# Optimization experiments

Measured on AMD Instinct MI355X. Metric: run time of the kernel, lower is better.

## Reference

```python
import jax, jax.numpy as jnp
import numpy as np
from math import factorial

N_NODES = 10000
N_EDGES = 320000
FEAT = 32
NBASIS = 8
RMAX = 6.0
ZMAX = 119


def _cg(j1, m1, j2, m2, j3, m3):
    if m1 + m2 != m3 or j3 < abs(j1 - j2) or j3 > j1 + j2:
        return 0.0
    f = lambda n: float(factorial(n))
    pre = ((2 * j3 + 1) * f(j1 + j2 - j3) * f(j1 - j2 + j3) * f(-j1 + j2 + j3) / f(j1 + j2 + j3 + 1)) ** 0.5
    pre *= (f(j3 + m3) * f(j3 - m3) * f(j1 - m1) * f(j1 + m1) * f(j2 - m2) * f(j2 + m2)) ** 0.5
    s = 0.0
    for k in range(j1 + j2 + j3 + 1):
        d = [k, j1 + j2 - j3 - k, j1 - m1 - k, j2 + m2 - k, j3 - j2 + m1 + k, j3 - j1 - m2 + k]
        if min(d) < 0:
            continue
        s += (-1) ** k / (f(d[0]) * f(d[1]) * f(d[2]) * f(d[3]) * f(d[4]) * f(d[5]))
    return pre * s


def _u_real(l):
    # complex->real spherical harmonics unitary transform
    U = np.zeros((2 * l + 1, 2 * l + 1), dtype=complex)
    s2 = 1.0 / np.sqrt(2.0)
    for m in range(-l, l + 1):
        i = m + l
        if m == 0:
            U[i, l] = 1.0
        elif m > 0:
            U[i, l + m] = ((-1) ** m) * s2
            U[i, l - m] = s2
        else:
            U[i, l + m] = 1j * s2
            U[i, l - m] = -1j * ((-1) ** m) * s2
    return U


def _real_cg():
    # real Clebsch-Gordan coupling coefficients for l<=2, shape (9,9,9), sparse
    off = [0, 1, 4]
    C = np.zeros((9, 9, 9))
    Us = [_u_real(l) for l in range(3)]
    for l1 in range(3):
        for l2 in range(3):
            for l3 in range(3):
                if l3 < abs(l1 - l2) or l3 > l1 + l2:
                    continue
                cg = np.zeros((2 * l1 + 1, 2 * l2 + 1, 2 * l3 + 1))
                for m1 in range(-l1, l1 + 1):
                    for m2 in range(-l2, l2 + 1):
                        m3 = m1 + m2
                        if abs(m3) <= l3:
                            cg[m1 + l1, m2 + l2, m3 + l3] = _cg(l1, m1, l2, m2, l3, m3)
                blk = np.einsum('ia,jb,kc,abc->ijk', Us[l1], Us[l2], np.conj(Us[l3]), cg.astype(complex))
                C[off[l1]:off[l1] + 2 * l1 + 1, off[l2]:off[l2] + 2 * l2 + 1, off[l3]:off[l3] + 2 * l3 + 1] = blk.real + blk.imag
    return C

CGC = jnp.asarray(_real_cg(), dtype=jnp.float32)
SL = [slice(0, 1), slice(1, 4), slice(4, 9)]
PATHS0 = [(0, 0, 0), (0, 1, 1), (0, 2, 2)]
PATHS1 = [(l1, l2, l3) for l1 in range(3) for l2 in range(3) for l3 in range(3) if abs(l1 - l2) <= l3 <= l1 + l2]
PATHS2 = [(0, 0, 0), (1, 1, 0), (2, 2, 0)]


def _real_sph(u):
    x, y, z = u[:, 0], u[:, 1], u[:, 2]
    c0 = 0.28209479177387814
    c1 = 0.4886025119029199
    c2a = 1.0925484305920792
    c2b = 0.31539156525252005
    c2c = 0.5462742152960396
    return jnp.stack([c0 * jnp.ones_like(x), c1 * y, c1 * z, c1 * x,
                      c2a * x * y, c2a * y * z, c2b * (3.0 * z * z - 1.0), c2a * x * z,
                      c2c * (x * x - y * y)], axis=-1)


def _message_pass(x, rad, Y, src, dst, W, paths, out_dim, n_nodes):
    # gather src node features -> per-edge CG tensor product with (radial x Ylm) basis -> scatter-add to dst
    xs = x[src, 0]  # (E, Dx, F)
    msg = jnp.zeros((rad.shape[0], out_dim, x.shape[-1]), x.dtype)
    for p, (l1, l2, l3) in enumerate(paths):
        w = rad @ W[p]  # (E, F) learned radial path weights
        contrib = jnp.einsum('abc,eaf,eb,ef->ecf', CGC[SL[l1], SL[l2], SL[l3]], xs[:, SL[l1], :], Y[:, SL[l2]], w)
        msg = msg.at[:, SL[l3], :].add(contrib)
    y = jax.ops.segment_sum(msg, dst, num_segments=n_nodes)
    return y[:, None]  # (N, 1, out_dim, F)


def _eadd(a, b):
    if a.shape[2] == b.shape[2]:
        return a + b
    if a.shape[2] < b.shape[2]:
        a, b = b, a
    return a.at[:, :, :b.shape[2], :].add(b)


def _edense(x, K, b):
    # equivariant Dense: shared kernel across degrees, bias only on scalar (l=0) channel
    y = jnp.einsum('npdf,fg->npdg', x, K)
    return y.at[:, :, 0, :].add(b)


def _esilu(x):
    # silu on scalars, sigmoid(scalar)-gated scaling on l>0 components (equivariant)
    if x.shape[2] == 1:
        return jax.nn.silu(x)
    s = x[:, :, 0:1, :]
    return jnp.concatenate([jax.nn.silu(s), x[:, :, 1:, :] * jax.nn.sigmoid(s)], axis=2)


def _forward(dr_vec, Z, neighbor_idxs, embed, wmp0, wmp1, wmp2, dk1, db1, dk2, db2):
    idx_i, idx_j = neighbor_idxs[0], neighbor_idxs[1]
    nN = Z.shape[0]
    r = jnp.sqrt(jnp.sum(dr_vec * dr_vec, axis=-1) + 1e-12)  # (E,)
    u = dr_vec / r[:, None]
    n = jnp.arange(1, NBASIS + 1, dtype=dr_vec.dtype)
    rad = jnp.sqrt(2.0 / RMAX) * jnp.sin(n * jnp.pi * r[:, None] / RMAX) / r[:, None]  # Bessel radial basis
    t = jnp.clip(r / RMAX, 0.0, 1.0 - 1e-6)
    cut = jnp.where(r < RMAX, jnp.exp(1.0 - 1.0 / (1.0 - t * t)), 0.0)  # smooth cutoff
    mask = (idx_i != idx_j).astype(dr_vec.dtype)  # mask padding/self edges
    rad = rad * (cut * mask)[:, None]
    Y = _real_sph(u)  # (E, 9)
    x = embed[Z][:, None, None, :]  # (N, 1, 1, F)
    for it, (paths, W) in enumerate([(PATHS0, wmp0), (PATHS1, wmp1), (PATHS2, wmp2)]):
        last = it == 2
        y = _message_pass(x, rad, Y, idx_j, idx_i, W, paths, 1 if last else 9, nN)
        if last:
            x = x[:, :, 0:1, :]  # change_max_degree_or_type -> scalars only
        y = _eadd(x, y)
        y = _edense(y, dk1[it], db1[it])
        y = _esilu(y)
        y = _edense(y, dk2[it], db2[it])
        x = _eadd(x, y)
    return x[:, 0, 0, :]


def setup_inputs():
    key = jax.random.key(0)
    ks = jax.random.split(key, 10)
    dr_vec = 2.0 * jax.random.normal(ks[0], (N_EDGES, 3), jnp.float32)
    Z = jax.random.randint(ks[1], (N_NODES,), 0, ZMAX)
    neighbor_idxs = jax.random.randint(ks[2], (2, N_EDGES), 0, N_NODES)
    embed = jax.random.normal(ks[3], (ZMAX, FEAT), jnp.float32)
    sB = 1.0 / np.sqrt(NBASIS)
    wmp0 = sB * jax.random.normal(ks[4], (len(PATHS0), NBASIS, FEAT), jnp.float32)
    wmp1 = sB * jax.random.normal(ks[5], (len(PATHS1), NBASIS, FEAT), jnp.float32)
    wmp2 = sB * jax.random.normal(ks[6], (len(PATHS2), NBASIS, FEAT), jnp.float32)
    sF = 1.0 / np.sqrt(FEAT)
    dense_k1 = sF * jax.random.normal(ks[7], (3, FEAT, FEAT), jnp.float32)
    dense_b1 = jnp.zeros((3, FEAT), jnp.float32)
    dense_k2 = 0.1 * sF * jax.random.normal(ks[8], (3, FEAT, FEAT), jnp.float32)
    dense_b2 = jnp.zeros((3, FEAT), jnp.float32)
    return {"dr_vec": dr_vec, "Z": Z, "neighbor_idxs": neighbor_idxs, "embed": embed,
            "wmp0": wmp0, "wmp1": wmp1, "wmp2": wmp2,
            "dense_k1": dense_k1, "dense_b1": dense_b1, "dense_k2": dense_k2, "dense_b2": dense_b2}


def reference(dr_vec, Z, neighbor_idxs, embed, wmp0, wmp1, wmp2, dense_k1, dense_b1, dense_k2, dense_b2):
    return _forward(dr_vec, Z, neighbor_idxs, embed, wmp0, wmp1, wmp2, dense_k1, dense_b1, dense_k2, dense_b2)
```

## Files before the change

kernel.cpp:

```cpp
#include <hip/hip_runtime.h>
#include <type_traits>
#include <cstdint>
#include <cstddef>

#define N_FEAT 32
#define NBASIS 8
#define SPAN   16
#define BSLOTS 8
#define BEDGES (SPAN*BSLOTS)

namespace cgc {

constexpr double dfact(int n){ double r=1.0; for(int i=2;i<=n;++i) r*=(double)i; return r; }

constexpr double dsqrt(double x){
  if(x<=0.0) return 0.0;
  double g = x>1.0 ? x : 1.0;
  for(int i=0;i<200;++i){ double ng = 0.5*(g + x/g); if(ng==g) break; g=ng; }
  return g;
}

constexpr double cg1(int j1,int m1,int j2,int m2,int j3,int m3){
  int adiff = j1-j2; if(adiff<0) adiff=-adiff;
  if(m1+m2!=m3 || j3<adiff || j3>j1+j2) return 0.0;
  double pre = dsqrt((double)(2*j3+1)*dfact(j1+j2-j3)*dfact(j1-j2+j3)*dfact(-j1+j2+j3)/dfact(j1+j2+j3+1));
  pre = pre*dsqrt(dfact(j3+m3)*dfact(j3-m3)*dfact(j1-m1)*dfact(j1+m1)*dfact(j2-m2)*dfact(j2+m2));
  double s=0.0;
  for(int k=0;k<=j1+j2+j3;++k){
    int d1=j1+j2-j3-k, d2=j1-m1-k, d3=j2+m2-k, d4=j3-j2+m1+k, d5=j3-j1-m2+k;
    if(d1<0||d2<0||d3<0||d4<0||d5<0) continue;
    double term = 1.0/(dfact(k)*dfact(d1)*dfact(d2)*dfact(d3)*dfact(d4)*dfact(d5));
    s += (k&1)? -term : term;
  }
  return pre*s;
}

struct Tab { float v[9][9][9]; };

constexpr Tab make(){
  Tab T{};
  int off[3]={0,1,4};
  double Ure[3][5][5]={}, Uim[3][5][5]={};
  const double s2 = dsqrt(0.5);
  for(int l=0;l<3;++l){
    for(int m=-l;m<=l;++m){
      int i=m+l;
      if(m==0){ Ure[l][i][l]=1.0; }
      else if(m>0){
        Ure[l][i][l+m] = ((m&1)? -1.0:1.0)*s2;
        Ure[l][i][l-m] = s2;
      } else {
        int am=-m;
        Uim[l][i][l+m] = s2;
        Uim[l][i][l-m] = -(((am&1)?-1.0:1.0))*s2;
      }
    }
  }
  for(int l1=0;l1<3;++l1) for(int l2=0;l2<3;++l2) for(int l3=0;l3<3;++l3){
    int lo = l1-l2; if(lo<0) lo=-lo;
    if(l3<lo || l3>l1+l2) continue;
    int d1=2*l1+1, d2=2*l2+1, d3=2*l3+1;
    double cg[5][5][5]={};
    for(int m1=-l1;m1<=l1;++m1) for(int m2=-l2;m2<=l2;++m2){
      int m3=m1+m2;
      if(m3>=-l3 && m3<=l3) cg[m1+l1][m2+l2][m3+l3] = cg1(l1,m1,l2,m2,l3,m3);
    }
    double t1re[5][5][5]={}, t1im[5][5][5]={};
    for(int a=0;a<d1;++a) for(int b=0;b<d2;++b) for(int k=0;k<d3;++k){
      double sre=0, sim=0;
      for(int c=0;c<d3;++c){
        double g=cg[a][b][c]; if(g==0.0) continue;
        sre += g*Ure[l3][k][c];
        sim -= g*Uim[l3][k][c];
      }
      t1re[a][b][k]=sre; t1im[a][b][k]=sim;
    }
    double t2re[5][5][5]={}, t2im[5][5][5]={};
    for(int a=0;a<d1;++a) for(int j=0;j<d2;++j) for(int k=0;k<d3;++k){
      double sre=0,sim=0;
      for(int b=0;b<d2;++b){
        double ur=Ure[l2][j][b], ui=Uim[l2][j][b];
        if(ur==0.0&&ui==0.0) continue;
        sre += ur*t1re[a][b][k]-ui*t1im[a][b][k];
        sim += ur*t1im[a][b][k]+ui*t1re[a][b][k];
      }
      t2re[a][j][k]=sre; t2im[a][j][k]=sim;
    }
    for(int i=0;i<d1;++i) for(int j=0;j<d2;++j) for(int k=0;k<d3;++k){
      double sre=0,sim=0;
      for(int a=0;a<d1;++a){
        double ur=Ure[l1][i][a], ui=Uim[l1][i][a];
        if(ur==0.0&&ui==0.0) continue;
        sre += ur*t2re[a][j][k]-ui*t2im[a][j][k];
        sim += ur*t2im[a][j][k]+ui*t2re[a][j][k];
      }
      T.v[off[l1]+i][off[l2]+j][off[l3]+k] = (float)(sre+sim);
    }
  }
  return T;
}

constexpr Tab T = make();

}

template<int I, int N, typename F>
__device__ __forceinline__ void sfor(F&& f){
  if constexpr (I < N){
    f(std::integral_constant<int,I>{});
    sfor<I+1,N>(static_cast<F&&>(f));
  }
}

constexpr int LOFF[3] = {0,1,4};

struct PS0 {
  static constexpr int NP=3;
  static constexpr int L[3][3]={{0,0,0},{0,1,1},{0,2,2}};
  static constexpr int ALO=0, AHI=1, OD=9, WOFF=0;
  static constexpr int MINW=4, DEPTH=8;
};
struct PS1a {
  static constexpr int NP=9;
  static constexpr int L[9][3]={{0,0,0},{0,1,1},{0,2,2},
                                {1,0,1},{1,1,0},{1,1,1},{1,1,2},{1,2,1},{1,2,2}};
  static constexpr int ALO=0, AHI=4, OD=9, WOFF=0;
  static constexpr int MINW=3, DEPTH=3;
};
struct PS1b {
  static constexpr int NP=6;
  static constexpr int L[6][3]={{2,0,2},{2,1,1},{2,1,2},{2,2,0},{2,2,1},{2,2,2}};
  static constexpr int ALO=4, AHI=9, OD=9, WOFF=9*NBASIS*N_FEAT;
  static constexpr int MINW=3, DEPTH=3;
};
struct PS2 {
  static constexpr int NP=3;
  static constexpr int L[3][3]={{0,0,0},{1,1,0},{2,2,0}};
  static constexpr int ALO=0, AHI=9, OD=1, WOFF=0;
  static constexpr int MINW=3, DEPTH=3;
};

__global__ void init_kernel(const float* __restrict__ embed, const int* __restrict__ Z,
                            float* __restrict__ xA, int* __restrict__ cnt, int nN){
  int i = blockIdx.x*256 + threadIdx.x;
  if(i >= nN*N_FEAT) return;
  int n = i>>5, f = i&31;
  if(f==0) cnt[n]=0;
  xA[(size_t)n*288 + f] = embed[Z[n]*N_FEAT + f];
}

__global__ void count_kernel(const int* __restrict__ dst, int* __restrict__ cnt, int E){
  int e = blockIdx.x*256 + threadIdx.x;
  if(e<E) atomicAdd(&cnt[dst[e]], 1);
}

__global__ void __launch_bounds__(1024) scan_kernel(const int* __restrict__ cnt,
                                                    int* __restrict__ cursor, int n){
  __shared__ int part[1024];
  const int tid = threadIdx.x;
  const int chunk = (n + 1023) >> 10;
  const int s0 = tid*chunk;
  const int s1 = (s0+chunk < n) ? s0+chunk : n;
  int s=0;
  for(int i=s0;i<s1;++i) s += cnt[i];
  part[tid]=s; __syncthreads();
  for(int off=1; off<1024; off<<=1){
    int v = 0;
    if(tid>=off) v = part[tid-off];
    __syncthreads();
    part[tid] += v;
    __syncthreads();
  }
  int run = part[tid] - s;
  for(int i=s0;i<s1;++i){
    int cv = cnt[i];
    cursor[i]=run;
    run += cv;
  }
}

__global__ void fillgeom_kernel(const int* __restrict__ dst, const int* __restrict__ src,
                                const float* __restrict__ dr, int* __restrict__ cursor,
                                int* __restrict__ srcsP, float* __restrict__ radY, int E){
  int e = blockIdx.x*256 + threadIdx.x;
  if(e>=E) return;
  const int d = dst[e], s = src[e];
  const int pos = atomicAdd(&cursor[d], 1);
  srcsP[pos] = s | (d<<16);

  float dx=dr[3*e], dy=dr[3*e+1], dz=dr[3*e+2];
  float r2 = fmaf(dx,dx,fmaf(dy,dy,fmaf(dz,dz,1e-12f)));
  float r = sqrtf(r2);
  float inv = 1.f/r;
  float ux=dx*inv, uy=dy*inv, uz=dz*inv;
  float t = r*(1.f/6.f);
  t = fminf(fmaxf(t,0.f), 1.f-1e-6f);
  float cut = 0.f;
  if (r < 6.f) cut = __expf(1.f - 1.f/(1.f - t*t));
  if (d==s) cut = 0.f;
  float base = 0.57735026918962576f * inv * cut;
  float* o = radY + (size_t)pos*20;
  const float pir = 0.52359877559829887f * r;
  float sT, cT;
  __sincosf(pir, &sT, &cT);
  const float twoc = 2.f*cT;
  float sp = 0.f, sc = sT;
  o[0] = base*sc;
  #pragma unroll
  for(int nb=2; nb<=8; ++nb){
    float sn = fmaf(twoc, sc, -sp);
    o[nb-1] = base*sn;
    sp = sc; sc = sn;
  }
  o[8]  = 0.28209479177387814f;
  o[9]  = 0.4886025119029199f*uy;
  o[10] = 0.4886025119029199f*uz;
  o[11] = 0.4886025119029199f*ux;
  o[12] = 1.0925484305920792f*ux*uy;
  o[13] = 1.0925484305920792f*uy*uz;
  o[14] = 0.31539156525252005f*(3.f*uz*uz-1.f);
  o[15] = 1.0925484305920792f*ux*uz;
  o[16] = 0.5462742152960396f*(ux*ux-uy*uy);
  o[17]=0.f; o[18]=0.f; o[19]=0.f;
}

template<class PS>
__device__ __forceinline__ void mp_body(
    int bid, float* sRad, int* sS,
    const int* __restrict__ srcsP, const float* __restrict__ radY,
    const float* __restrict__ x_in, const float* __restrict__ W,
    float* __restrict__ ymsg, int E)
{
  constexpr int NP = PS::NP;
  constexpr int ALO = PS::ALO, AHI = PS::AHI, DA = AHI-ALO;
  constexpr int OD = PS::OD;
  constexpr int DEPTH = PS::DEPTH, NBUF = DEPTH+1;

  const int tid  = threadIdx.x;
  const int base = bid * BEDGES;
  const int nE   = (base + BEDGES <= E) ? BEDGES : (E - base);

  {
    const float4* g4 = (const float4*)(radY + (size_t)base*20);
    float4* s4 = (float4*)sRad;
    const int n4 = nE*5;
    for (int i=tid; i<n4; i+=256) s4[i] = g4[i];
    for (int i=tid; i<nE;  i+=256) sS[i] = srcsP[base+i];
  }
  __syncthreads();

  const int f  = tid & 31;
  const int k0 = (tid>>5)*SPAN;
  if (k0 >= nE) return;

  float Wreg[NP][NBASIS];
  sfor<0,NP>([&](auto P){
    sfor<0,NBASIS>([&](auto Q){
      Wreg[P.value][Q.value] = W[PS::WOFF + (P.value*NBASIS+Q.value)*N_FEAT + f];
    });
  });

  float msg[OD];
  sfor<0,OD>([&](auto C){ msg[C.value]=0.f; });

  auto gather = [&](float (&dst)[DA], int k){
    const int s = sS[k] & 0xFFFF;
    const float* xb = x_in + (size_t)s*288 + ALO*N_FEAT + f;
    sfor<0,DA>([&](auto A){ dst[A.value] = xb[A.value*N_FEAT]; });
  };

  auto compute = [&](const float (&xs)[DA], int k){
    const float* rp = sRad + k*20;
    const float4 q0 = *(const float4*)(rp);
    const float4 q1 = *(const float4*)(rp+4);
    const float4 q2 = *(const float4*)(rp+8);
    const float4 q3 = *(const float4*)(rp+12);
    const float y8 = rp[16];
    const float rad[8] = {q0.x,q0.y,q0.z,q0.w,q1.x,q1.y,q1.z,q1.w};
    const float Yv[9]  = {q2.x,q2.y,q2.z,q2.w,q3.x,q3.y,q3.z,q3.w,y8};
    sfor<0,NP>([&](auto P){
      constexpr int p  = P.value;
      constexpr int l1 = PS::L[p][0], l2 = PS::L[p][1], l3 = PS::L[p][2];
      constexpr int o1 = LOFF[l1], o2 = LOFF[l2], o3 = LOFF[l3];
      float w = 0.f;
      sfor<0,NBASIS>([&](auto Q){ w = fmaf(rad[Q.value], Wreg[p][Q.value], w); });
      sfor<0,2*l2+1>([&](auto B){
        constexpr int b = B.value;
        const float yw = Yv[o2+b]*w;
        sfor<0,2*l1+1>([&](auto A){
          constexpr int a = A.value;
          sfor<0,2*l3+1>([&](auto C){
            constexpr int c = C.value;
            constexpr float cgv = cgc::T.v[o1+a][o2+b][o3+c];
            if constexpr (cgv > 1e-7f || cgv < -1e-7f){
              msg[o3+c] = fmaf(cgv*xs[o1+a-ALO], yw, msg[o3+c]);
            }
          });
        });
      });
    });
  };

  auto flush = [&](int d){
    float* yb = ymsg + ((size_t)d*OD)*N_FEAT + f;
    sfor<0,OD>([&](auto C){
      atomicAdd(yb + C.value*N_FEAT, msg[C.value]);
      msg[C.value] = 0.f;
    });
  };

  if (nE == BEDGES){
    float buf[NBUF][DA];
    sfor<0,DEPTH>([&](auto J){ gather(buf[J.value], k0 + J.value); });
    int vcur = sS[k0];
    sfor<0,SPAN>([&](auto I){
      constexpr int i = I.value;
      int vnext;
      if constexpr (i+1 < SPAN) vnext = sS[k0+i+1]; else vnext = -1;
      if constexpr (i+DEPTH < SPAN) gather(buf[(i+DEPTH)%NBUF], k0+i+DEPTH);
      compute(buf[i%NBUF], k0+i);
      if (i == SPAN-1 || (vnext>>16) != (vcur>>16)) flush(vcur>>16);
      vcur = vnext;
    });
  } else {
    const int k1 = (k0+SPAN < nE) ? k0+SPAN : nE;
    for (int k=k0; k<k1; ++k){
      float xs[DA];
      gather(xs, k);
      compute(xs, k);
      const int dc = sS[k]>>16;
      const int dn = (k+1 < k1) ? (sS[k+1]>>16) : -1;
      if (dn != dc) flush(dc);
    }
  }
}

template<class PS>
__global__ void __launch_bounds__(256, PS::MINW) mp_kernel(
    const int* __restrict__ srcsP, const float* __restrict__ radY,
    const float* __restrict__ x_in, const float* __restrict__ W,
    float* __restrict__ ymsg, int E)
{
  __shared__ float sRad[BEDGES*20];
  __shared__ int   sS[BEDGES];
  mp_body<PS>(blockIdx.x, sRad, sS, srcsP, radY, x_in, W, ymsg, E);
}

template<int DX>
__global__ void __launch_bounds__(256) nodeA_kernel(
    const float* __restrict__ xin, const float* __restrict__ ymsg,
    const float* __restrict__ K1, const float* __restrict__ b1,
    const float* __restrict__ K2, const float* __restrict__ b2,
    float* __restrict__ xout, int nN)
{
  __shared__ float sK1[1024], sK2[1024], sb1[32], sb2[32];
  __shared__ float tb[8][9][32];
  const int tid = threadIdx.x;
  for(int i=tid;i<1024;i+=256){ sK1[i]=K1[i]; sK2[i]=K2[i]; }
  if(tid<32){ sb1[tid]=b1[tid]; sb2[tid]=b2[tid]; }
  __syncthreads();
  const int h = tid>>5, f = tid&31;
  const int n = blockIdx.x*8 + h;
  const bool valid = n < nN;
  const int nc = valid ? n : 0;
  float xi[9];
  #pragma unroll
  for(int c=0;c<9;++c){
    float t = ymsg[((size_t)nc*9+c)*32+f];
    float x = 0.f;
    if (c<DX) x = xin[((size_t)nc*9+c)*32+f];
    xi[c]=x;
    tb[h][c][f] = t + x;
  }
  __syncthreads();
  float u[9];
  #pragma unroll
  for(int c=0;c<9;++c){
    float acc = (c==0) ? sb1[f] : 0.f;
    #pragma unroll
    for(int g=0;g<32;++g) acc = fmaf(tb[h][c][g], sK1[g*32+f], acc);
    u[c]=acc;
  }
  const float gate = 1.f/(1.f+expf(-u[0]));
  __syncthreads();
  #pragma unroll
  for(int c=0;c<9;++c) tb[h][c][f] = u[c]*gate;
  __syncthreads();
  #pragma unroll
  for(int c=0;c<9;++c){
    float acc = (c==0) ? sb2[f] : 0.f;
    #pragma unroll
    for(int g=0;g<32;++g) acc = fmaf(tb[h][c][g], sK2[g*32+f], acc);
    if (valid) xout[((size_t)n*9+c)*32+f] = acc + ((c<DX) ? xi[c] : 0.f);
  }
}

__global__ void __launch_bounds__(256) nodeB_kernel(
    const float* __restrict__ xin, const float* __restrict__ msg0,
    const float* __restrict__ K1, const float* __restrict__ b1,
    const float* __restrict__ K2, const float* __restrict__ b2,
    float* __restrict__ out, int nN)
{
  __shared__ float sK1[1024], sK2[1024], sb1[32], sb2[32];
  __shared__ float tb[8][32];
  const int tid = threadIdx.x;
  for(int i=tid;i<1024;i+=256){ sK1[i]=K1[i]; sK2[i]=K2[i]; }
  if(tid<32){ sb1[tid]=b1[tid]; sb2[tid]=b2[tid]; }
  __syncthreads();
  const int h = tid>>5, f = tid&31;
  const int n = blockIdx.x*8 + h;
  const bool valid = n < nN;
  const int nc = valid ? n : 0;
  const float x0 = xin[(size_t)nc*288 + f];
  tb[h][f] = msg0[(size_t)nc*32+f] + x0;
  __syncthreads();
  float acc = sb1[f];
  #pragma unroll
  for(int g=0;g<32;++g) acc = fmaf(tb[h][g], sK1[g*32+f], acc);
  const float gate = 1.f/(1.f+expf(-acc));
  const float v = acc*gate;
  __syncthreads();
  tb[h][f] = v;
  __syncthreads();
  float acc2 = sb2[f];
  #pragma unroll
  for(int g=0;g<32;++g) acc2 = fmaf(tb[h][g], sK2[g*32+f], acc2);
  if (valid) out[(size_t)n*32+f] = x0 + acc2;
}

extern "C" void kernel_launch(void* const* d_in, const int* in_sizes, int n_in,
                              void* d_out, int out_size, void* d_ws, size_t ws_size,
                              hipStream_t stream) {
  const float* dr    = (const float*)d_in[0];
  const int*   Z     = (const int*)  d_in[1];
  const int*   nbr   = (const int*)  d_in[2];
  const float* embed = (const float*)d_in[3];
  const float* wmp0  = (const float*)d_in[4];
  const float* wmp1  = (const float*)d_in[5];
  const float* wmp2  = (const float*)d_in[6];
  const float* dk1   = (const float*)d_in[7];
  const float* db1   = (const float*)d_in[8];
  const float* dk2   = (const float*)d_in[9];
  const float* db2   = (const float*)d_in[10];
  const int nN = in_sizes[1];
  const int E  = in_sizes[2]/2;
  const int* idx_i = nbr;
  const int* idx_j = nbr + E;

  uintptr_t base = (uintptr_t)d_ws;
  auto alloc = [&](size_t bytes)->void*{
    uintptr_t p = (base + 255) & ~(uintptr_t)255;
    base = p + bytes;
    return (void*)p;
  };
  float* radY    = (float*)alloc((size_t)E*20*4);
  int*   cnt     = (int*)  alloc((size_t)nN*4);
  int*   cursor  = (int*)  alloc((size_t)nN*4);
  int*   srcsP   = (int*)  alloc((size_t)E*4);
  float* xA      = (float*)alloc((size_t)nN*288*4);
  float* xB      = (float*)alloc((size_t)nN*288*4);
  float* ymsg    = (float*)alloc((size_t)nN*288*4);

  const int gE  = (E+255)/256;
  const int gI  = (nN*N_FEAT+255)/256;
  const int gND = (nN+7)/8;
  const int gMP = (E + BEDGES - 1) / BEDGES;
  const size_t ymsgBytes = (size_t)nN*288*4;

  init_kernel    <<<gI, 256, 0, stream>>>(embed, Z, xA, cnt, nN);
  count_kernel   <<<gE, 256, 0, stream>>>(idx_i, cnt, E);
  scan_kernel    <<<1, 1024, 0, stream>>>(cnt, cursor, nN);
  fillgeom_kernel<<<gE, 256, 0, stream>>>(idx_i, idx_j, dr, cursor, srcsP, radY, E);

  hipMemsetAsync(ymsg, 0, ymsgBytes, stream);
  mp_kernel<PS0><<<gMP, 256, 0, stream>>>(srcsP, radY, xA, wmp0, ymsg, E);
  nodeA_kernel<1><<<gND, 256, 0, stream>>>(xA, ymsg, dk1, db1, dk2, db2, xB, nN);
  hipMemsetAsync(ymsg, 0, ymsgBytes, stream);
  mp_kernel<PS1a><<<gMP, 256, 0, stream>>>(srcsP, radY, xB, wmp1, ymsg, E);
  mp_kernel<PS1b><<<gMP, 256, 0, stream>>>(srcsP, radY, xB, wmp1, ymsg, E);
  nodeA_kernel<9><<<gND, 256, 0, stream>>>(xB, ymsg, dk1+1024, db1+32, dk2+1024, db2+32, xA, nN);
  hipMemsetAsync(ymsg, 0, (size_t)nN*32*4, stream);
  mp_kernel<PS2><<<gMP, 256, 0, stream>>>(srcsP, radY, xA, wmp2, ymsg, E);
  nodeB_kernel<<<gND, 256, 0, stream>>>(xA, ymsg, dk1+2048, db1+64, dk2+2048, db2+64,
                                        (float*)d_out, nN);
}
```

Before: 426.7 us.

## Pack radial/SH table to 16 floats and merge layer-1 message kernels

Drops the constant Y00 entry and the padding from the per-edge radial/spherical-harmonic record, shrinking it from 20 to 16 floats. The Y00 constant is instead folded into the weights of l2=0 paths at load time. This cuts global traffic and shared-memory footprint per block. The two layer-1 message-passing launches are also merged into one kernel whose block index selects the path subset, which removes a launch boundary and lets both halves run concurrently. The merged kernel must hold the code for both templates, so register allocation may change.

```diff
diff --git a/kernel.cpp b/kernel.cpp
--- a/kernel.cpp
+++ b/kernel.cpp
@@ -113,6 +113,7 @@
 }
 
 constexpr int LOFF[3] = {0,1,4};
+constexpr float Y0C = 0.28209479177387814f;
 
 struct PS0 {
   static constexpr int NP=3;
@@ -199,7 +200,7 @@
   if (r < 6.f) cut = __expf(1.f - 1.f/(1.f - t*t));
   if (d==s) cut = 0.f;
   float base = 0.57735026918962576f * inv * cut;
-  float* o = radY + (size_t)pos*20;
+  float* o = radY + (size_t)pos*16;
   const float pir = 0.52359877559829887f * r;
   float sT, cT;
   __sincosf(pir, &sT, &cT);
@@ -212,16 +213,14 @@
     o[nb-1] = base*sn;
     sp = sc; sc = sn;
   }
-  o[8]  = 0.28209479177387814f;
-  o[9]  = 0.4886025119029199f*uy;
-  o[10] = 0.4886025119029199f*uz;
-  o[11] = 0.4886025119029199f*ux;
-  o[12] = 1.0925484305920792f*ux*uy;
-  o[13] = 1.0925484305920792f*uy*uz;
-  o[14] = 0.31539156525252005f*(3.f*uz*uz-1.f);
-  o[15] = 1.0925484305920792f*ux*uz;
-  o[16] = 0.5462742152960396f*(ux*ux-uy*uy);
-  o[17]=0.f; o[18]=0.f; o[19]=0.f;
+  o[8]  = 0.4886025119029199f*uy;
+  o[9]  = 0.4886025119029199f*uz;
+  o[10] = 0.4886025119029199f*ux;
+  o[11] = 1.0925484305920792f*ux*uy;
+  o[12] = 1.0925484305920792f*uy*uz;
+  o[13] = 0.31539156525252005f*(3.f*uz*uz-1.f);
+  o[14] = 1.0925484305920792f*ux*uz;
+  o[15] = 0.5462742152960396f*(ux*ux-uy*uy);
 }
 
 template<class PS>
@@ -241,9 +240,9 @@
   const int nE   = (base + BEDGES <= E) ? BEDGES : (E - base);
 
   {
-    const float4* g4 = (const float4*)(radY + (size_t)base*20);
+    const float4* g4 = (const float4*)(radY + (size_t)base*16);
     float4* s4 = (float4*)sRad;
-    const int n4 = nE*5;
+    const int n4 = nE*4;
     for (int i=tid; i<n4; i+=256) s4[i] = g4[i];
     for (int i=tid; i<nE;  i+=256) sS[i] = srcsP[base+i];
   }
@@ -255,8 +254,12 @@
 
   float Wreg[NP][NBASIS];
   sfor<0,NP>([&](auto P){
+    constexpr int p = P.value;
+    constexpr bool fold = (PS::L[p][1]==0);
     sfor<0,NBASIS>([&](auto Q){
-      Wreg[P.value][Q.value] = W[PS::WOFF + (P.value*NBASIS+Q.value)*N_FEAT + f];
+      float v = W[PS::WOFF + (p*NBASIS+Q.value)*N_FEAT + f];
+      if constexpr (fold) v *= Y0C;
+      Wreg[p][Q.value] = v;
     });
   });
 
@@ -270,14 +273,13 @@
   };
 
   auto compute = [&](const float (&xs)[DA], int k){
-    const float* rp = sRad + k*20;
+    const float* rp = sRad + k*16;
     const float4 q0 = *(const float4*)(rp);
     const float4 q1 = *(const float4*)(rp+4);
     const float4 q2 = *(const float4*)(rp+8);
     const float4 q3 = *(const float4*)(rp+12);
-    const float y8 = rp[16];
     const float rad[8] = {q0.x,q0.y,q0.z,q0.w,q1.x,q1.y,q1.z,q1.w};
-    const float Yv[9]  = {q2.x,q2.y,q2.z,q2.w,q3.x,q3.y,q3.z,q3.w,y8};
+    const float Yv[8]  = {q2.x,q2.y,q2.z,q2.w,q3.x,q3.y,q3.z,q3.w};
     sfor<0,NP>([&](auto P){
       constexpr int p  = P.value;
       constexpr int l1 = PS::L[p][0], l2 = PS::L[p][1], l3 = PS::L[p][2];
@@ -286,7 +288,9 @@
       sfor<0,NBASIS>([&](auto Q){ w = fmaf(rad[Q.value], Wreg[p][Q.value], w); });
       sfor<0,2*l2+1>([&](auto B){
         constexpr int b = B.value;
-        const float yw = Yv[o2+b]*w;
+        float yw;
+        if constexpr (l2==0) yw = w;
+        else                 yw = Yv[o2+b-1]*w;
         sfor<0,2*l1+1>([&](auto A){
           constexpr int a = A.value;
           sfor<0,2*l3+1>([&](auto C){
@@ -341,9 +345,21 @@
     const float* __restrict__ x_in, const float* __restrict__ W,
     float* __restrict__ ymsg, int E)
 {
-  __shared__ float sRad[BEDGES*20];
+  __shared__ float sRad[BEDGES*16];
   __shared__ int   sS[BEDGES];
   mp_body<PS>(blockIdx.x, sRad, sS, srcsP, radY, x_in, W, ymsg, E);
+}
+
+__global__ void __launch_bounds__(256, 3) mp1_kernel(
+    const int* __restrict__ srcsP, const float* __restrict__ radY,
+    const float* __restrict__ x_in, const float* __restrict__ W,
+    float* __restrict__ ymsg, int E, int gMP)
+{
+  __shared__ float sRad[BEDGES*16];
+  __shared__ int   sS[BEDGES];
+  const int b = blockIdx.x;
+  if (b < gMP) mp_body<PS1a>(b,     sRad, sS, srcsP, radY, x_in, W, ymsg, E);
+  else         mp_body<PS1b>(b-gMP, sRad, sS, srcsP, radY, x_in, W, ymsg, E);
 }
 
 template<int DX>
@@ -453,7 +469,7 @@
     base = p + bytes;
     return (void*)p;
   };
-  float* radY    = (float*)alloc((size_t)E*20*4);
+  float* radY    = (float*)alloc((size_t)E*16*4);
   int*   cnt     = (int*)  alloc((size_t)nN*4);
   int*   cursor  = (int*)  alloc((size_t)nN*4);
   int*   srcsP   = (int*)  alloc((size_t)E*4);
@@ -476,8 +492,7 @@
   mp_kernel<PS0><<<gMP, 256, 0, stream>>>(srcsP, radY, xA, wmp0, ymsg, E);
   nodeA_kernel<1><<<gND, 256, 0, stream>>>(xA, ymsg, dk1, db1, dk2, db2, xB, nN);
   hipMemsetAsync(ymsg, 0, ymsgBytes, stream);
-  mp_kernel<PS1a><<<gMP, 256, 0, stream>>>(srcsP, radY, xB, wmp1, ymsg, E);
-  mp_kernel<PS1b><<<gMP, 256, 0, stream>>>(srcsP, radY, xB, wmp1, ymsg, E);
+  mp1_kernel<<<2*gMP, 256, 0, stream>>>(srcsP, radY, xB, wmp1, ymsg, E, gMP);
   nodeA_kernel<9><<<gND, 256, 0, stream>>>(xB, ymsg, dk1+1024, db1+32, dk2+1024, db2+32, xA, nN);
   hipMemsetAsync(ymsg, 0, (size_t)nN*32*4, stream);
   mp_kernel<PS2><<<gMP, 256, 0, stream>>>(srcsP, radY, xA, wmp2, ymsg, E);
```

Measured after the change: 409.0 us. 4.1% less time.
